# Optimization experiments

Hardware: AMD Instinct MI355X
Metric: run time of the kernel (lower is better)

Reference implementation:

```python
import jax, jax.numpy as jnp
import numpy as np
from jax import lax

EPS = 1e-5
K = 13  # correlation window (pad 6 each side)

def _conv(x, w, b):
    # 3x3 conv, stride 1, padding 1, NCHW/OIHW
    y = lax.conv_general_dilated(x, w, (1, 1), ((1, 1), (1, 1)),
                                 dimension_numbers=('NCHW', 'OIHW', 'NCHW'))
    return y + b[None, :, None, None]

def _inorm(x):
    # InstanceNorm2d: per-sample per-channel, biased var, no affine
    m = jnp.mean(x, axis=(2, 3), keepdims=True)
    v = jnp.mean((x - m) ** 2, axis=(2, 3), keepdims=True)
    return (x - m) * lax.rsqrt(v + EPS)

def _block(x, wa, ba, wb, bb):
    x = jax.nn.relu(_conv(x, wa, ba))
    x = jax.nn.relu(_conv(x, wb, bb))
    return _inorm(x)

def _forward(color, corr, w1a, b1a, w1b, b1b, w2a, b2a, w2b, b2b,
             w3a, b3a, w3b, b3b, w4a, b4a, w4b, b4b, H, W):
    conv1 = _block(color[:, :, ::2, ::2], w1a, b1a, w1b, b1b)   # (B,64,2H,2W)
    conv2 = _block(conv1[:, :, ::2, ::2], w2a, b2a, w2b, b2b)   # (B,128,H,W)
    B, C = conv2.shape[0], conv2.shape[1]
    pad = jnp.pad(conv2, ((0, 0), (0, 0), (6, 6), (6, 6)), mode='edge')
    # 'pre' mode: content-adaptive 13x13 windowed weighted sum.
    # accumulating corr[:, t] * shifted-window of conv2_pad.
    def body(acc, t):
        i, j = t // K, t % K
        patch = lax.dynamic_slice(pad, (0, 0, i, j), (B, C, H, W))
        acc = acc + corr[:, t][:, None, :] * patch.reshape(B, C, H * W)
        return acc, None
    align, _ = lax.scan(body, jnp.zeros((B, C, H * W), conv2.dtype),
                        jnp.arange(K * K))
    align_1 = align.reshape(B, C, H, W)                          # (B,128,H,W)
    align_2 = _block(align_1[:, :, ::2, ::2], w3a, b3a, w3b, b3b)  # (B,256,H/2,W/2)
    align_3 = _block(align_2[:, :, ::2, ::2], w4a, b4a, w4b, b4b)  # (B,512,H/4,W/4)
    return (align_1, align_2, align_3)

def setup_inputs() -> dict:
    key = jax.random.key(0)
    ks = jax.random.split(key, 20)
    def w(k, shape):
        return jax.random.normal(k, shape, jnp.float32) * 0.05
    B, H, W = 4, 128, 128
    inp = {
        'color': jax.random.normal(ks[0], (B, 2, 4 * H, 4 * W), jnp.float32),
        'corr': jax.random.normal(ks[1], (B, K * K, H * W), jnp.float32) * 0.05,
        'w1a': w(ks[2], (64, 2, 3, 3)),    'b1a': jnp.zeros((64,), jnp.float32),
        'w1b': w(ks[3], (64, 64, 3, 3)),   'b1b': jnp.zeros((64,), jnp.float32),
        'w2a': w(ks[4], (128, 64, 3, 3)),  'b2a': jnp.zeros((128,), jnp.float32),
        'w2b': w(ks[5], (128, 128, 3, 3)), 'b2b': jnp.zeros((128,), jnp.float32),
        'w3a': w(ks[6], (256, 128, 3, 3)), 'b3a': jnp.zeros((256,), jnp.float32),
        'w3b': w(ks[7], (256, 256, 3, 3)), 'b3b': jnp.zeros((256,), jnp.float32),
        'w4a': w(ks[8], (512, 256, 3, 3)), 'b4a': jnp.zeros((512,), jnp.float32),
        'w4b': w(ks[9], (512, 512, 3, 3)), 'b4b': jnp.zeros((512,), jnp.float32),
        'H': H, 'W': W,
    }
    return inp

def reference(color, corr, w1a, b1a, w1b, b1b, w2a, b2a, w2b, b2b,
              w3a, b3a, w3b, b3b, w4a, b4a, w4b, b4b, H, W):
    return _forward(color, corr, w1a, b1a, w1b, b1b, w2a, b2a, w2b, b2b,
                    w3a, b3a, w3b, b3b, w4a, b4a, w4b, b4b, H, W)
```

## Files before the change

kernel.cpp:

```cpp
#include <hip/hip_runtime.h>
#include <hip/hip_bf16.h>

typedef __hip_bfloat16 bf16;
typedef __attribute__((ext_vector_type(8))) short short8;
typedef __attribute__((ext_vector_type(4))) float f32x4;

__device__ __forceinline__ float b2f(bf16 v) { return __bfloat162float(v); }
__device__ __forceinline__ bf16 f2b(float v) { return __float2bfloat16(v); }
__device__ __forceinline__ short fbits(float v) {
  bf16 h = f2b(v); return *reinterpret_cast<short*>(&h);
}
__device__ __forceinline__ float sb2f(short s) {
  return b2f(*reinterpret_cast<bf16*>(&s));
}
__device__ __forceinline__ int xcd_swz(int bid, int nwg) {
  int q = nwg >> 3, r = nwg & 7;
  int xcd = bid & 7, idx = bid >> 3;
  return (xcd < r ? xcd * (q + 1) : r * (q + 1) + (xcd - r) * q) + idx;
}

__global__ __launch_bounds__(256) void repack_k(
    const float* __restrict__ w, short* __restrict__ Wr, int Cin, int Cout)
{
  const int nkc = Cin >> 5, ncof = Cout >> 4;
  const size_t gid = (size_t)blockIdx.x * 256 + threadIdx.x;
  const int lane = gid & 63;
  size_t r = gid >> 6;
  const int tap = r % 9; r /= 9;
  const int kcc = r % nkc; r /= nkc;
  const int cof = r % ncof;
  const int hl = r / ncof;
  const int co = cof * 16 + (lane & 15);
  short8 v;
#pragma unroll
  for (int j = 0; j < 8; ++j) {
    int ci = kcc * 32 + ((lane >> 4) * 8 + j);
    float wv = w[((size_t)co * Cin + ci) * 9 + tap];
    bf16 hi = f2b(wv);
    v[j] = hl ? fbits(wv - b2f(hi)) : *reinterpret_cast<short*>(&hi);
  }
  *reinterpret_cast<short8*>(Wr + gid * 8) = v;
}

template<int R, int CX, int S>
__global__ __launch_bounds__(256) void conv_mfma_k(
    const bf16* __restrict__ src, bf16* __restrict__ dst,
    const short8* __restrict__ Wr, const float* __restrict__ bias,
    const float2* __restrict__ stats,
    int Win, int Hout, int Wout, int Cin, int Cout, int XT)
{
  constexpr int ROWS = R + 2;
  constexpr int COLS = CX + 2;
  constexpr int NGR = ROWS * 4 * COLS;
  constexpr int FM = (R * CX) / 32;
  __shared__ short8 a_s[NGR];

  const int ytn = Hout / R;
  const int nxy = XT * ytn;
  const int wg = xcd_swz(blockIdx.x, gridDim.x);
  const int cog = wg / (4 * nxy);
  const int rem = wg - cog * (4 * nxy);
  const int b = rem / nxy;
  const int pxb = rem - b * nxy;
  const int xt = pxb % XT, yt = pxb / XT;
  const int x0 = xt * CX, y0 = yt * R;

  const int tid = threadIdx.x, lane = tid & 63, wid = tid >> 6;
  const int wm = wid & 1, wn = wid >> 1;
  const int nkc = Cin >> 5;
  const int ncof = Cout >> 4;
  const int l15 = lane & 15, lg = lane >> 4;

  f32x4 acc[FM][2] = {};

  int arow[FM], acolb[FM];
#pragma unroll
  for (int fm = 0; fm < FM; ++fm) {
    int p = wm * (R * CX / 2) + fm * 16 + l15;
    arow[fm] = p / CX;
    acolb[fm] = p % CX;
  }

  auto bload = [&](int hl, int fn, int kcc, int tap) -> short8 {
    int cof = cog * 4 + wn * 2 + fn;
    return Wr[((((size_t)hl * ncof + cof) * nkc + kcc) * 9 + tap) * 64 + lane];
  };

  short8 bc[2][2], bn_[2][2];
  bc[0][0] = bload(0, 0, 0, 0); bc[0][1] = bload(0, 1, 0, 0);
  bc[1][0] = bload(1, 0, 0, 0); bc[1][1] = bload(1, 1, 0, 0);

  for (int kc = 0; kc < nkc; ++kc) {
    __syncthreads();
    for (int idx = tid; idx < NGR; idx += 256) {
      int g = idx & 3, cix = idx >> 2;
      int col = cix % COLS, row = cix / COLS;
      int sy = y0 + row - 1;
      int sx = x0 + col - 1;
      short8 v = {};
      if (sy >= 0 && sy < Hout && sx >= 0 && sx < Wout) {
        int ry = S ? 2 * sy : sy, rx = S ? 2 * sx : sx;
        v = *reinterpret_cast<const short8*>(
            reinterpret_cast<const short*>(src) +
            (((size_t)b * (S ? 2 * Hout : Hout) + ry) * Win + rx) * Cin +
            kc * 32 + g * 8);
        if (stats) {
          const float2* st = stats + (size_t)b * Cin + kc * 32 + g * 8;
#pragma unroll
          for (int j = 0; j < 8; ++j)
            v[j] = fbits((sb2f(v[j]) - st[j].x) * st[j].y);
        }
      }
      a_s[(row * 4 + g) * COLS + col] = v;
    }
    __syncthreads();

#pragma unroll
    for (int tap = 0; tap < 9; ++tap) {
      const int dy = tap / 3, dx = tap % 3;
      int nt = tap + 1, nk = kc;
      if (nt == 9) { nt = 0; nk = (kc + 1 < nkc) ? kc + 1 : 0; }
      bn_[0][0] = bload(0, 0, nk, nt); bn_[0][1] = bload(0, 1, nk, nt);
      bn_[1][0] = bload(1, 0, nk, nt); bn_[1][1] = bload(1, 1, nk, nt);
#pragma unroll
      for (int fm = 0; fm < FM; ++fm) {
        short8 a = a_s[((arow[fm] + dy) * 4 + lg) * COLS + acolb[fm] + dx];
        acc[fm][0] = __builtin_amdgcn_mfma_f32_16x16x32_bf16(a, bc[0][0], acc[fm][0], 0, 0, 0);
        acc[fm][0] = __builtin_amdgcn_mfma_f32_16x16x32_bf16(a, bc[1][0], acc[fm][0], 0, 0, 0);
        acc[fm][1] = __builtin_amdgcn_mfma_f32_16x16x32_bf16(a, bc[0][1], acc[fm][1], 0, 0, 0);
        acc[fm][1] = __builtin_amdgcn_mfma_f32_16x16x32_bf16(a, bc[1][1], acc[fm][1], 0, 0, 0);
      }
      bc[0][0] = bn_[0][0]; bc[0][1] = bn_[0][1];
      bc[1][0] = bn_[1][0]; bc[1][1] = bn_[1][1];
    }
  }

#pragma unroll
  for (int fn = 0; fn < 2; ++fn) {
    int co = cog * 64 + wn * 32 + fn * 16 + l15;
    float bs = bias[co];
#pragma unroll
    for (int fm = 0; fm < FM; ++fm) {
#pragma unroll
      for (int j = 0; j < 4; ++j) {
        int p = wm * (R * CX / 2) + fm * 16 + lg * 4 + j;
        int r = p / CX, x = p % CX;
        float v = fmaxf(acc[fm][fn][j] + bs, 0.f);
        dst[((size_t)(b * Hout + y0 + r) * Wout + x0 + x) * Cout + co] = f2b(v);
      }
    }
  }
}

__global__ __launch_bounds__(256) void conv1a_k(
    const float* __restrict__ src, bf16* __restrict__ dst,
    const float* __restrict__ w, const float* __restrict__ bias)
{
  const int b = blockIdx.z, cog = blockIdx.y;
  const int ty0 = (blockIdx.x / 16) * 16, tx0 = (blockIdx.x % 16) * 16;
  const int tid = threadIdx.x, tx = tid & 15, ty = tid >> 4;

  __shared__ float in_s[2][18][18];
  __shared__ __align__(16) float w_s[2][3][3][16];

  for (int idx = tid; idx < 2 * 324; idx += 256) {
    int ci = idx / 324, r = idx - ci * 324;
    int iy = r / 18, ix = r - iy * 18;
    int gy = ty0 + iy - 1, gx = tx0 + ix - 1;
    float v = 0.f;
    if (gy >= 0 && gy < 256 && gx >= 0 && gx < 256)
      v = src[((size_t)(b * 2 + ci) * 512 + 2 * gy) * 512 + 2 * gx];
    in_s[ci][iy][ix] = v;
  }
  for (int idx = tid; idx < 2 * 144; idx += 256) {
    int co = idx & 15, r = idx >> 4;
    int ci = r / 9, k = r - ci * 9;
    w_s[ci][k / 3][k % 3][co] = w[(size_t)((cog * 16 + co) * 2 + ci) * 9 + k];
  }
  __syncthreads();

  float acc[16];
#pragma unroll
  for (int i = 0; i < 16; ++i) acc[i] = 0.f;
  for (int ci = 0; ci < 2; ++ci)
#pragma unroll
    for (int dy = 0; dy < 3; ++dy)
#pragma unroll
      for (int dx = 0; dx < 3; ++dx) {
        float v = in_s[ci][ty + dy][tx + dx];
        const float4* wv = (const float4*)(&w_s[ci][dy][dx][0]);
        float4 w0 = wv[0], w1 = wv[1], w2 = wv[2], w3 = wv[3];
        acc[0] = fmaf(v, w0.x, acc[0]);   acc[1] = fmaf(v, w0.y, acc[1]);
        acc[2] = fmaf(v, w0.z, acc[2]);   acc[3] = fmaf(v, w0.w, acc[3]);
        acc[4] = fmaf(v, w1.x, acc[4]);   acc[5] = fmaf(v, w1.y, acc[5]);
        acc[6] = fmaf(v, w1.z, acc[6]);   acc[7] = fmaf(v, w1.w, acc[7]);
        acc[8] = fmaf(v, w2.x, acc[8]);   acc[9] = fmaf(v, w2.y, acc[9]);
        acc[10] = fmaf(v, w2.z, acc[10]); acc[11] = fmaf(v, w2.w, acc[11]);
        acc[12] = fmaf(v, w3.x, acc[12]); acc[13] = fmaf(v, w3.y, acc[13]);
        acc[14] = fmaf(v, w3.z, acc[14]); acc[15] = fmaf(v, w3.w, acc[15]);
      }

  const int gy = ty0 + ty, gx = tx0 + tx;
  short8 s0, s1;
#pragma unroll
  for (int j = 0; j < 8; ++j) {
    s0[j] = fbits(fmaxf(acc[j] + bias[cog * 16 + j], 0.f));
    s1[j] = fbits(fmaxf(acc[8 + j] + bias[cog * 16 + 8 + j], 0.f));
  }
  short8* dp = reinterpret_cast<short8*>(
      reinterpret_cast<short*>(dst) + (((size_t)(b * 256 + gy) * 256 + gx) * 64 + cog * 16));
  dp[0] = s0; dp[1] = s1;
}

__global__ __launch_bounds__(256) void inorm_stats1_k(
    const bf16* __restrict__ x, float2* __restrict__ part,
    int HW, int C, int nb, int PC)
{
  const int b = blockIdx.y, pc = blockIdx.x;
  const int NC8 = C >> 3;
  const int pgc = 256 / NC8;
  const int c8 = (threadIdx.x % NC8) * 8;
  const int pg = threadIdx.x / NC8;
  const int chunk = HW / PC;
  const int p0 = pc * chunk;

  float s[8] = {}, ss[8] = {};
  for (int p = p0 + pg; p < p0 + chunk; p += pgc) {
    short8 v = *reinterpret_cast<const short8*>(
        reinterpret_cast<const short*>(x) + ((size_t)b * HW + p) * C + c8);
#pragma unroll
    for (int j = 0; j < 8; ++j) {
      float f = sb2f(v[j]);
      s[j] += f; ss[j] += f * f;
    }
  }
  __shared__ float sh[2][2048];
#pragma unroll
  for (int j = 0; j < 8; ++j) {
    sh[0][pg * C + c8 + j] = s[j];
    sh[1][pg * C + c8 + j] = ss[j];
  }
  __syncthreads();
  for (int c = threadIdx.x; c < C; c += 256) {
    float as = 0.f, aq = 0.f;
    for (int g = 0; g < pgc; ++g) { as += sh[0][g * C + c]; aq += sh[1][g * C + c]; }
    part[((size_t)pc * nb + b) * C + c] = make_float2(as, aq);
  }
}

__global__ __launch_bounds__(256) void inorm_stats2_k(
    const float2* __restrict__ part, float2* __restrict__ stats,
    int HW, int C, int PC, int nb)
{
  const int b = blockIdx.y, cg = blockIdx.x;
  const int c = threadIdx.x & 63, i = threadIdx.x >> 6;
  float s = 0.f, ss = 0.f;
  for (int pc = i; pc < PC; pc += 4) {
    float2 v = part[((size_t)pc * nb + b) * C + cg * 64 + c];
    s += v.x; ss += v.y;
  }
  __shared__ float sh[2][4][64];
  sh[0][i][c] = s; sh[1][i][c] = ss;
  __syncthreads();
  if (threadIdx.x < 64) {
    int cc = threadIdx.x;
    float s4 = sh[0][0][cc] + sh[0][1][cc] + sh[0][2][cc] + sh[0][3][cc];
    float q4 = sh[1][0][cc] + sh[1][1][cc] + sh[1][2][cc] + sh[1][3][cc];
    float m = s4 / (float)HW;
    float var = q4 / (float)HW - m * m;
    stats[(size_t)b * C + cg * 64 + cc] = make_float2(m, rsqrtf(var + 1e-5f));
  }
}

__global__ __launch_bounds__(256) void inorm_apply_k(
    const bf16* __restrict__ x, const float2* __restrict__ stats, int HW, int C,
    bf16* __restrict__ dnhwc, float* __restrict__ fnchw)
{
  const int b = blockIdx.z, cg = blockIdx.y;
  const int c = cg * 64 + (threadIdx.x & 63);
  const int p = blockIdx.x * 4 + (threadIdx.x >> 6);
  const float2 st = stats[(size_t)b * C + c];
  const size_t ia = ((size_t)b * HW + p) * C + c;
  const float v = (b2f(x[ia]) - st.x) * st.y;
  if (dnhwc) dnhwc[ia] = f2b(v);
  if (fnchw) fnchw[((size_t)(b * C + c)) * HW + p] = v;
}

__global__ __launch_bounds__(256) void inorm_apply_pad_k(
    const bf16* __restrict__ x, const float2* __restrict__ stats,
    bf16* __restrict__ pad)
{
  const int b = blockIdx.z, cg = blockIdx.y, yy = blockIdx.x;
  const int tid = threadIdx.x;
  __shared__ bf16 t_s[64][130];
  __shared__ float2 st_s[64];
  if (tid < 64) st_s[tid] = stats[(size_t)b * 128 + cg * 64 + tid];
  __syncthreads();

  const int c8 = (tid & 7) * 8, px0 = tid >> 3;
#pragma unroll
  for (int pass = 0; pass < 4; ++pass) {
    int px = pass * 32 + px0;
    short8 v = *reinterpret_cast<const short8*>(
        reinterpret_cast<const short*>(x) +
        ((size_t)(b * 16384 + yy * 128 + px) * 128 + cg * 64 + c8));
#pragma unroll
    for (int j = 0; j < 8; ++j) {
      float2 st = st_s[c8 + j];
      t_s[c8 + j][px] = f2b((sb2f(v[j]) - st.x) * st.y);
    }
  }
  __syncthreads();

  for (int idx = tid; idx < 64 * 18; idx += 256) {
    int c = idx / 18, g = idx - (idx / 18) * 18;
    short8 v;
#pragma unroll
    for (int j = 0; j < 8; ++j) {
      int xx = g * 8 + j - 6;
      xx = xx < 0 ? 0 : (xx > 127 ? 127 : xx);
      v[j] = *reinterpret_cast<short*>(&t_s[c][xx]);
    }
    *reinterpret_cast<short8*>(
        reinterpret_cast<short*>(pad) +
        ((size_t)(b * 128 + cg * 64 + c) * 128 + yy) * 144 + g * 8) = v;
  }
}

__global__ __launch_bounds__(256) void corr_mfma_k(
    const float* __restrict__ corr, const bf16* __restrict__ pad,
    float* __restrict__ outc, bf16* __restrict__ outn, int b0)
{
  __shared__ __align__(16) char smem[26 * 64 * 16];
  short8* a_lds = reinterpret_cast<short8*>(smem);
  float* out_s = reinterpret_cast<float*>(smem);

  const int b = b0 + blockIdx.z;
  const int wg = xcd_swz(blockIdx.x, gridDim.x);
  const int y = wg >> 3, xt = wg & 7;
  const int x0 = xt * 16;
  const int tid = threadIdx.x, lane = tid & 63, wid = tid >> 6;
  const int l15 = lane & 15, lg = lane >> 4;

  for (int idx = tid; idx < 26 * 64; idx += 256) {
    short8 z = {};
    a_lds[idx] = z;
  }
  __syncthreads();

  unsigned short* ah = reinterpret_cast<unsigned short*>(a_lds);
  for (int idx = tid; idx < 169 * 16; idx += 256) {
    int t = idx >> 4, m = idx & 15;
    int dy = t / 13, dx = t - dy * 13;
    float f = corr[((size_t)b * 169 + t) * 16384 + y * 128 + x0 + m];
    bf16 hi = f2b(f);
    unsigned short hb = *reinterpret_cast<unsigned short*>(&hi);
    unsigned short lb = (unsigned short)fbits(f - b2f(hi));
    int k = m + dx;
    int ent = dy * 64 + (k >> 3) * 16 + m;
    ah[ent * 8 + (k & 7)] = hb;
    ah[(13 * 64 + ent) * 8 + (k & 7)] = lb;
  }
  __syncthreads();

  const int cg0 = wid * 2;
  f32x4 acc0 = {}, acc1 = {};
  const short* pb = reinterpret_cast<const short*>(pad);

  for (int dy = 0; dy < 13; ++dy) {
    int rowc = y + dy - 6; rowc = rowc < 0 ? 0 : (rowc > 127 ? 127 : rowc);
    short8 bhi = a_lds[dy * 64 + lane];
    short8 blo = a_lds[(13 + dy) * 64 + lane];
    size_t base0 = ((size_t)(b * 128 + cg0 * 16 + l15) * 128 + rowc) * 144
                   + x0 + lg * 8;
    short8 a0 = *reinterpret_cast<const short8*>(pb + base0);
    short8 a1 = *reinterpret_cast<const short8*>(pb + base0 + (size_t)16 * 128 * 144);
    acc0 = __builtin_amdgcn_mfma_f32_16x16x32_bf16(a0, bhi, acc0, 0, 0, 0);
    acc1 = __builtin_amdgcn_mfma_f32_16x16x32_bf16(a1, bhi, acc1, 0, 0, 0);
    acc0 = __builtin_amdgcn_mfma_f32_16x16x32_bf16(a0, blo, acc0, 0, 0, 0);
    acc1 = __builtin_amdgcn_mfma_f32_16x16x32_bf16(a1, blo, acc1, 0, 0, 0);
  }
  __syncthreads();

#pragma unroll
  for (int cgi = 0; cgi < 2; ++cgi) {
    f32x4 a = cgi ? acc1 : acc0;
    float* dst4 = out_s + l15 * 132 + (cg0 + cgi) * 16 + lg * 4;
    *reinterpret_cast<f32x4*>(dst4) = a;
  }
  __syncthreads();

  {
    int px_ = tid >> 4, c8 = (tid & 15) * 8;
    const float* row = out_s + px_ * 132 + c8;
    short8 v;
#pragma unroll
    for (int j = 0; j < 8; ++j) v[j] = fbits(row[j]);
    *reinterpret_cast<short8*>(
        reinterpret_cast<short*>(outn) +
        ((size_t)(b * 16384 + y * 128 + x0 + px_)) * 128 + c8) = v;
  }
  {
    int ch = tid >> 1, pg = tid & 1;
    float v0[4], v1[4];
#pragma unroll
    for (int i = 0; i < 4; ++i) v0[i] = out_s[(pg * 8 + i) * 132 + ch];
#pragma unroll
    for (int i = 0; i < 4; ++i) v1[i] = out_s[(pg * 8 + 4 + i) * 132 + ch];
    float* dst = outc + ((size_t)(b * 128 + ch)) * 16384 + y * 128 + x0 + pg * 8;
    *reinterpret_cast<float4*>(dst) = make_float4(v0[0], v0[1], v0[2], v0[3]);
    *reinterpret_cast<float4*>(dst + 4) = make_float4(v1[0], v1[1], v1[2], v1[3]);
  }
}

extern "C" void kernel_launch(void* const* d_in, const int* in_sizes, int n_in,
                              void* d_out, int out_size, void* d_ws, size_t ws_size,
                              hipStream_t stream) {
  const float* color = (const float*)d_in[0];
  const float* corr  = (const float*)d_in[1];
  const float* w1a = (const float*)d_in[2];  const float* b1a = (const float*)d_in[3];
  const float* w1b = (const float*)d_in[4];  const float* b1b = (const float*)d_in[5];
  const float* w2a = (const float*)d_in[6];  const float* b2a = (const float*)d_in[7];
  const float* w2b = (const float*)d_in[8];  const float* b2b = (const float*)d_in[9];
  const float* w3a = (const float*)d_in[10]; const float* b3a = (const float*)d_in[11];
  const float* w3b = (const float*)d_in[12]; const float* b3b = (const float*)d_in[13];
  const float* w4a = (const float*)d_in[14]; const float* b4a = (const float*)d_in[15];
  const float* w4b = (const float*)d_in[16]; const float* b4b = (const float*)d_in[17];

  float* out = (float*)d_out;
  char* ws = (char*)d_ws;
  const size_t MB = 1048576;
  float2* stats = (float2*)ws;
  float2* part  = (float2*)(ws + (64 << 10));
  short*  WrS   = (short*)(ws + (256 << 10));
  const short8* Wr = (const short8*)WrS;
  bf16* P0 = (bf16*)(ws + 10 * MB);
  bf16* P1 = (bf16*)(ws + 27 * MB);
  bf16* P2 = (bf16*)(ws + 44 * MB);
  bf16* X1 = P0;
  bf16* X2 = (bf16*)d_out;
  const float2* nost = (const float2*)nullptr;

  conv1a_k<<<dim3(256, 4, 4), 256, 0, stream>>>(color, X1, w1a, b1a);
  repack_k<<<36, 256, 0, stream>>>(w1b, WrS, 64, 64);
  conv_mfma_k<16, 16, 0><<<1024, 256, 0, stream>>>(
      X1, X2, Wr, b1b, nost, 256, 256, 256, 64, 64, 16);
  inorm_stats1_k<<<dim3(64, 4), 256, 0, stream>>>(X2, part, 65536, 64, 4, 64);
  inorm_stats2_k<<<dim3(1, 4), 256, 0, stream>>>(part, stats, 65536, 64, 64, 4);

  repack_k<<<72, 256, 0, stream>>>(w2a, WrS, 64, 128);
  conv_mfma_k<16, 16, 1><<<512, 256, 0, stream>>>(
      X2, P0, Wr, b2a, stats, 256, 128, 128, 64, 128, 8);
  repack_k<<<144, 256, 0, stream>>>(w2b, WrS, 128, 128);
  conv_mfma_k<16, 16, 0><<<512, 256, 0, stream>>>(
      P0, P1, Wr, b2b, nost, 128, 128, 128, 128, 128, 8);
  inorm_stats1_k<<<dim3(64, 4), 256, 0, stream>>>(P1, part, 16384, 128, 4, 64);
  inorm_stats2_k<<<dim3(2, 4), 256, 0, stream>>>(part, stats, 16384, 128, 64, 4);
  inorm_apply_pad_k<<<dim3(128, 2, 4), 256, 0, stream>>>(P1, stats, P2);

  corr_mfma_k<<<dim3(128 * 8, 1, 2), 256, 0, stream>>>(corr, P2, out, P0, 0);
  corr_mfma_k<<<dim3(128 * 8, 1, 2), 256, 0, stream>>>(corr, P2, out, P0, 2);

  repack_k<<<288, 256, 0, stream>>>(w3a, WrS, 128, 256);
  conv_mfma_k<8, 16, 1><<<512, 256, 0, stream>>>(
      P0, P1, Wr, b3a, nost, 128, 64, 64, 128, 256, 4);
  repack_k<<<576, 256, 0, stream>>>(w3b, WrS, 256, 256);
  conv_mfma_k<8, 16, 0><<<512, 256, 0, stream>>>(
      P1, P2, Wr, b3b, nost, 64, 64, 64, 256, 256, 4);
  inorm_stats1_k<<<dim3(32, 4), 256, 0, stream>>>(P2, part, 4096, 256, 4, 32);
  inorm_stats2_k<<<dim3(4, 4), 256, 0, stream>>>(part, stats, 4096, 256, 32, 4);
  inorm_apply_k<<<dim3(1024, 4, 4), 256, 0, stream>>>(
      P2, stats, 4096, 256, (bf16*)nullptr, out + 8388608);

  repack_k<<<1152, 256, 0, stream>>>(w4a, WrS, 256, 512);
  conv_mfma_k<4, 16, 1><<<512, 256, 0, stream>>>(
      P2, P1, Wr, b4a, stats, 64, 32, 32, 256, 512, 2);
  repack_k<<<2304, 256, 0, stream>>>(w4b, WrS, 512, 512);
  conv_mfma_k<4, 16, 0><<<512, 256, 0, stream>>>(
      P1, P2, Wr, b4b, nost, 32, 32, 32, 512, 512, 2);
  inorm_stats1_k<<<dim3(32, 4), 256, 0, stream>>>(P2, part, 1024, 512, 4, 32);
  inorm_stats2_k<<<dim3(8, 4), 256, 0, stream>>>(part, stats, 1024, 512, 32, 4);
  inorm_apply_k<<<dim3(256, 8, 4), 256, 0, stream>>>(
      P2, stats, 1024, 512, (bf16*)nullptr, out + 12582912);
}
```

Measured before the change: 487.7 us.

## Split-K the two deepest convolutions with fp32 partials and a combine kernel

After: 489.6 us. No clear change (+0.4%).

```diff
diff --git a/kernel.cpp b/kernel.cpp
--- a/kernel.cpp
+++ b/kernel.cpp
@@ -46,8 +46,8 @@
 __global__ __launch_bounds__(256) void conv_mfma_k(
     const bf16* __restrict__ src, bf16* __restrict__ dst,
     const short8* __restrict__ Wr, const float* __restrict__ bias,
-    const float2* __restrict__ stats,
-    int Win, int Hout, int Wout, int Cin, int Cout, int XT)
+    const float2* __restrict__ stats, float* __restrict__ pout,
+    int Win, int Hout, int Wout, int Cin, int Cout, int XT, int KS)
 {
   constexpr int ROWS = R + 2;
   constexpr int COLS = CX + 2;
@@ -57,9 +57,12 @@
 
   const int ytn = Hout / R;
   const int nxy = XT * ytn;
+  const int ncog = Cout >> 6;
   const int wg = xcd_swz(blockIdx.x, gridDim.x);
-  const int cog = wg / (4 * nxy);
-  const int rem = wg - cog * (4 * nxy);
+  const int ks = wg / (ncog * 4 * nxy);
+  const int rem2 = wg - ks * (ncog * 4 * nxy);
+  const int cog = rem2 / (4 * nxy);
+  const int rem = rem2 - cog * (4 * nxy);
   const int b = rem / nxy;
   const int pxb = rem - b * nxy;
   const int xt = pxb % XT, yt = pxb / XT;
@@ -68,6 +71,8 @@
   const int tid = threadIdx.x, lane = tid & 63, wid = tid >> 6;
   const int wm = wid & 1, wn = wid >> 1;
   const int nkc = Cin >> 5;
+  const int nkcs = nkc / KS;
+  const int kc0 = ks * nkcs;
   const int ncof = Cout >> 4;
   const int l15 = lane & 15, lg = lane >> 4;
 
@@ -87,10 +92,10 @@
   };
 
   short8 bc[2][2], bn_[2][2];
-  bc[0][0] = bload(0, 0, 0, 0); bc[0][1] = bload(0, 1, 0, 0);
-  bc[1][0] = bload(1, 0, 0, 0); bc[1][1] = bload(1, 1, 0, 0);
-
-  for (int kc = 0; kc < nkc; ++kc) {
+  bc[0][0] = bload(0, 0, kc0, 0); bc[0][1] = bload(0, 1, kc0, 0);
+  bc[1][0] = bload(1, 0, kc0, 0); bc[1][1] = bload(1, 1, kc0, 0);
+
+  for (int kc = kc0; kc < kc0 + nkcs; ++kc) {
     __syncthreads();
     for (int idx = tid; idx < NGR; idx += 256) {
       int g = idx & 3, cix = idx >> 2;
@@ -119,7 +124,7 @@
     for (int tap = 0; tap < 9; ++tap) {
       const int dy = tap / 3, dx = tap % 3;
       int nt = tap + 1, nk = kc;
-      if (nt == 9) { nt = 0; nk = (kc + 1 < nkc) ? kc + 1 : 0; }
+      if (nt == 9) { nt = 0; nk = (kc + 1 < kc0 + nkcs) ? kc + 1 : kc0; }
       bn_[0][0] = bload(0, 0, nk, nt); bn_[0][1] = bload(0, 1, nk, nt);
       bn_[1][0] = bload(1, 0, nk, nt); bn_[1][1] = bload(1, 1, nk, nt);
 #pragma unroll
@@ -145,11 +150,33 @@
       for (int j = 0; j < 4; ++j) {
         int p = wm * (R * CX / 2) + fm * 16 + lg * 4 + j;
         int r = p / CX, x = p % CX;
-        float v = fmaxf(acc[fm][fn][j] + bs, 0.f);
-        dst[((size_t)(b * Hout + y0 + r) * Wout + x0 + x) * Cout + co] = f2b(v);
+        size_t oi = ((size_t)(b * Hout + y0 + r) * Wout + x0 + x) * Cout + co;
+        if (pout) {
+          pout[(size_t)ks * ((size_t)4 * Hout * Wout * Cout) + oi] = acc[fm][fn][j];
+        } else {
+          dst[oi] = f2b(fmaxf(acc[fm][fn][j] + bs, 0.f));
+        }
       }
     }
   }
+}
+
+__global__ __launch_bounds__(256) void combine2_k(
+    const float* __restrict__ p, const float* __restrict__ bias,
+    bf16* __restrict__ dst, int n4, int Cout)
+{
+  int i = blockIdx.x * 256 + threadIdx.x;
+  if (i >= n4) return;
+  float4 a = reinterpret_cast<const float4*>(p)[i];
+  float4 c = reinterpret_cast<const float4*>(p + (size_t)n4 * 4)[i];
+  int co = (i * 4) & (Cout - 1);
+  float4 bs = *reinterpret_cast<const float4*>(bias + co);
+  short v0 = fbits(fmaxf(a.x + c.x + bs.x, 0.f));
+  short v1 = fbits(fmaxf(a.y + c.y + bs.y, 0.f));
+  short v2 = fbits(fmaxf(a.z + c.z + bs.z, 0.f));
+  short v3 = fbits(fmaxf(a.w + c.w + bs.w, 0.f));
+  short4 pk = make_short4(v0, v1, v2, v3);
+  *reinterpret_cast<short4*>(reinterpret_cast<short*>(dst) + (size_t)i * 4) = pk;
 }
 
 __global__ __launch_bounds__(256) void conv1a_k(
@@ -437,23 +464,25 @@
   bf16* P0 = (bf16*)(ws + 10 * MB);
   bf16* P1 = (bf16*)(ws + 27 * MB);
   bf16* P2 = (bf16*)(ws + 44 * MB);
+  float* PK = (float*)(ws + 10 * MB);
   bf16* X1 = P0;
   bf16* X2 = (bf16*)d_out;
   const float2* nost = (const float2*)nullptr;
+  float* nop = (float*)nullptr;
 
   conv1a_k<<<dim3(256, 4, 4), 256, 0, stream>>>(color, X1, w1a, b1a);
   repack_k<<<36, 256, 0, stream>>>(w1b, WrS, 64, 64);
   conv_mfma_k<16, 16, 0><<<1024, 256, 0, stream>>>(
-      X1, X2, Wr, b1b, nost, 256, 256, 256, 64, 64, 16);
+      X1, X2, Wr, b1b, nost, nop, 256, 256, 256, 64, 64, 16, 1);
   inorm_stats1_k<<<dim3(64, 4), 256, 0, stream>>>(X2, part, 65536, 64, 4, 64);
   inorm_stats2_k<<<dim3(1, 4), 256, 0, stream>>>(part, stats, 65536, 64, 64, 4);
 
   repack_k<<<72, 256, 0, stream>>>(w2a, WrS, 64, 128);
   conv_mfma_k<16, 16, 1><<<512, 256, 0, stream>>>(
-      X2, P0, Wr, b2a, stats, 256, 128, 128, 64, 128, 8);
+      X2, P0, Wr, b2a, stats, nop, 256, 128, 128, 64, 128, 8, 1);
   repack_k<<<144, 256, 0, stream>>>(w2b, WrS, 128, 128);
   conv_mfma_k<16, 16, 0><<<512, 256, 0, stream>>>(
-      P0, P1, Wr, b2b, nost, 128, 128, 128, 128, 128, 8);
+      P0, P1, Wr, b2b, nost, nop, 128, 128, 128, 128, 128, 8, 1);
   inorm_stats1_k<<<dim3(64, 4), 256, 0, stream>>>(P1, part, 16384, 128, 4, 64);
   inorm_stats2_k<<<dim3(2, 4), 256, 0, stream>>>(part, stats, 16384, 128, 64, 4);
   inorm_apply_pad_k<<<dim3(128, 2, 4), 256, 0, stream>>>(P1, stats, P2);
@@ -463,21 +492,23 @@
 
   repack_k<<<288, 256, 0, stream>>>(w3a, WrS, 128, 256);
   conv_mfma_k<8, 16, 1><<<512, 256, 0, stream>>>(
-      P0, P1, Wr, b3a, nost, 128, 64, 64, 128, 256, 4);
+      P0, P1, Wr, b3a, nost, nop, 128, 64, 64, 128, 256, 4, 1);
   repack_k<<<576, 256, 0, stream>>>(w3b, WrS, 256, 256);
   conv_mfma_k<8, 16, 0><<<512, 256, 0, stream>>>(
-      P1, P2, Wr, b3b, nost, 64, 64, 64, 256, 256, 4);
+      P1, P2, Wr, b3b, nost, nop, 64, 64, 64, 256, 256, 4, 1);
   inorm_stats1_k<<<dim3(32, 4), 256, 0, stream>>>(P2, part, 4096, 256, 4, 32);
   inorm_stats2_k<<<dim3(4, 4), 256, 0, stream>>>(part, stats, 4096, 256, 32, 4);
   inorm_apply_k<<<dim3(1024, 4, 4), 256, 0, stream>>>(
       P2, stats, 4096, 256, (bf16*)nullptr, out + 8388608);
 
   repack_k<<<1152, 256, 0, stream>>>(w4a, WrS, 256, 512);
-  conv_mfma_k<4, 16, 1><<<512, 256, 0, stream>>>(
-      P2, P1, Wr, b4a, stats, 64, 32, 32, 256, 512, 2);
+  conv_mfma_k<4, 16, 1><<<1024, 256, 0, stream>>>(
+      P2, (bf16*)nullptr, Wr, b4a, stats, PK, 64, 32, 32, 256, 512, 2, 2);
+  combine2_k<<<2048, 256, 0, stream>>>(PK, b4a, P1, 524288, 512);
   repack_k<<<2304, 256, 0, stream>>>(w4b, WrS, 512, 512);
-  conv_mfma_k<4, 16, 0><<<512, 256, 0, stream>>>(
-      P1, P2, Wr, b4b, nost, 32, 32, 32, 512, 512, 2);
+  conv_mfma_k<4, 16, 0><<<1024, 256, 0, stream>>>(
+      P1, (bf16*)nullptr, Wr, b4b, nost, PK, 32, 32, 32, 512, 512, 2, 2);
+  combine2_k<<<2048, 256, 0, stream>>>(PK, b4b, P2, 524288, 512);
   inorm_stats1_k<<<dim3(32, 4), 256, 0, stream>>>(P2, part, 1024, 512, 4, 32);
   inorm_stats2_k<<<dim3(8, 4), 256, 0, stream>>>(part, stats, 1024, 512, 32, 4);
   inorm_apply_k<<<dim3(256, 8, 4), 256, 0, stream>>>(
```
